# Kernel optimization log

Measured on AMD Instinct MI355X. Metric: run time of the kernel, lower is better.

Reference implementation:

```python
import jax, jax.numpy as jnp
import numpy as np

N = 4096
E = 131072
IN_C, HID, HEADS, OUT_C = 512, 64, 8, 256
BETA = 0.5
NEG_SLOPE = 0.2


def _glorot(key, shape, fan_in, fan_out):
    lim = float(np.sqrt(6.0 / (fan_in + fan_out)))
    return jax.random.uniform(key, shape, jnp.float32, -lim, lim)


def setup_inputs() -> dict:
    key = jax.random.key(0)
    ks = jax.random.split(key, 12)
    x = jax.random.normal(ks[0], (N, IN_C), jnp.float32)
    src = jax.random.randint(ks[1], (E,), 0, N)
    dst = jax.random.randint(ks[2], (E,), 0, N)
    dst = jnp.where(src == dst, (dst + 1) % N, dst)  # no self loops (module removes then re-adds)
    edge_index = jnp.stack([src, dst]).astype(jnp.int64)
    # layer 1: in=512 -> heads=8, out=64 (concat -> 512), residual=False
    W1 = _glorot(ks[3], (IN_C, HEADS * HID), IN_C, HEADS * HID)
    as1 = _glorot(ks[4], (HEADS, HID), HID, HID)
    ad1 = _glorot(ks[5], (HEADS, HID), HID, HID)
    b1 = jnp.zeros((HEADS * HID,), jnp.float32)
    # layer 2: in=512 -> heads=1, out=256, concat=False, residual=True (res_linear needed)
    W2 = _glorot(ks[6], (HEADS * HID, OUT_C), HEADS * HID, OUT_C)
    as2 = _glorot(ks[7], (1, OUT_C), OUT_C, OUT_C)
    ad2 = _glorot(ks[8], (1, OUT_C), OUT_C, OUT_C)
    b2 = jnp.zeros((OUT_C,), jnp.float32)
    resW2 = _glorot(ks[9], (HEADS * HID, OUT_C), HEADS * HID, OUT_C)
    return {"x": x, "edge_index": edge_index, "W1": W1, "as1": as1, "ad1": ad1,
            "b1": b1, "W2": W2, "as2": as2, "ad2": ad2, "b2": b2, "resW2": resW2}


def _seg_softmax(e, seg, n):
    # numerically-stable softmax over edges grouped by destination node
    m = jax.ops.segment_max(e, seg, num_segments=n)  # [n, H]
    a = jnp.exp(e - m[seg])
    s = jax.ops.segment_sum(a, seg, num_segments=n)
    return a / (s[seg] + 1e-16)


def _motif_gat_layer(x, edge_index, W, a_src, a_dst, bias, res_W, heads, out_ch, concat):
    n = x.shape[0]
    residual = x
    h = (x @ W).reshape(n, heads, out_ch)
    # add self loops (input edge_index has none)
    loops = jnp.arange(n, dtype=edge_index.dtype)
    src = jnp.concatenate([edge_index[0], loops])
    dst = jnp.concatenate([edge_index[1], loops])
    xj = h[src]  # [E', H, C]
    xi = h[dst]
    e = (xj * a_src[None]).sum(-1) + (xi * a_dst[None]).sum(-1)  # [E', H]
    alpha_first = _seg_softmax(jax.nn.leaky_relu(e, NEG_SLOPE), dst, n)
    # motif adjacency: dense A^3, row-normalized by clamped row sum
    adj = jnp.zeros((n, n), x.dtype).at[src, dst].set(1.0)
    m3 = adj @ adj @ adj
    m3 = m3 / jnp.clip(m3.sum(-1, keepdims=True), 1.0)
    mw = m3[src, dst][:, None]  # [E', 1]
    alpha_motif = _seg_softmax(jax.nn.leaky_relu(e * mw, NEG_SLOPE), dst, n)
    alpha = BETA * alpha_first + (1.0 - BETA) * alpha_motif  # dropout: eval mode -> identity
    out = jax.ops.segment_sum(alpha[:, :, None] * xj, dst, num_segments=n)  # [n, H, C]
    out = out.reshape(n, heads * out_ch) if concat else out.mean(1)
    if res_W is not None:
        out = out + residual @ res_W
    return out + bias


def reference(x, edge_index, W1, as1, ad1, b1, W2, as2, ad2, b2, resW2):
    h = _motif_gat_layer(x, edge_index, W1, as1, ad1, b1, None, HEADS, HID, True)
    h = jax.nn.elu(h)  # dropout: eval mode -> identity
    out = _motif_gat_layer(h, edge_index, W2, as2, ad2, b2, resW2, 1, OUT_C, False)
    return out
```

## Files before the change

### kernel.cpp

```cpp
#include <hip/hip_runtime.h>
#include <hip/hip_bf16.h>
#include <math.h>

#define NN 4096
#define EE 131072
#define EP (EE + NN)
#define C1 512
#define H1 8
#define C2 256
#define NWORDS 128
#define KP 520

typedef __attribute__((ext_vector_type(8))) short bf16x8;
typedef __attribute__((ext_vector_type(4))) float f32x4;

__device__ __forceinline__ float wredMaxf(float v){
#pragma unroll
  for(int o=32;o;o>>=1) v = fmaxf(v, __shfl_xor(v,o));
  return v;
}
__device__ __forceinline__ float wredSumf(float v){
#pragma unroll
  for(int o=32;o;o>>=1) v += __shfl_xor(v,o);
  return v;
}
__device__ __forceinline__ int wredSumi(int v){
#pragma unroll
  for(int o=32;o;o>>=1) v += __shfl_xor(v,o);
  return v;
}

__device__ __forceinline__ void bfsplit(float v, unsigned short& h, unsigned short& l){
  unsigned bits = __float_as_uint(v);
  h = (unsigned short)(bits>>16);
  float hf = __uint_as_float(bits & 0xFFFF0000u);
  float lo = v - hf;
  l = (unsigned short)(__float_as_uint(lo)>>16);
}

__device__ __forceinline__ unsigned short f2bf_rne(float v){
  unsigned b = __float_as_uint(v);
  return (unsigned short)((b + 0x7FFFu + ((b>>16)&1u)) >> 16);
}

__device__ __forceinline__ int detect_mode(const int* __restrict__ ei32){
  unsigned nz = 0;
#pragma unroll
  for(int i=1;i<16;i+=2) nz |= (unsigned)ei32[i];
  return nz != 0;
}

__device__ __forceinline__ void edge_sd(const int* ei32, int mode, int e, int& s, int& d){
  if(e < EE){
    if(mode==0){ s = ei32[2*e]; d = ei32[2*(EE+e)]; }
    else       { s = ei32[e];   d = ei32[EE+e]; }
  } else { s = e - EE; d = s; }
}

__global__ __launch_bounds__(256) void k_build_cvt(const int* __restrict__ ei32,
    unsigned* __restrict__ rowbits, unsigned* __restrict__ colbits, unsigned* __restrict__ cnt,
    const float* __restrict__ X, unsigned short* __restrict__ xh, unsigned short* __restrict__ xl,
    const float* __restrict__ W1f, const float* __restrict__ W2f, const float* __restrict__ Wrf,
    unsigned short* __restrict__ b1h, unsigned short* __restrict__ b1l,
    unsigned short* __restrict__ b2h, unsigned short* __restrict__ b2l){
  int b = blockIdx.x, t = threadIdx.x;
  if(b < 528){
    int e = b*256 + t;
    if(e >= EP) return;
    int m = detect_mode(ei32), s, d;
    edge_sd(ei32, m, e, s, d);
    atomicOr(&rowbits[s*NWORDS + (d>>5)], 1u<<(d&31));
    atomicOr(&colbits[d*NWORDS + (s>>5)], 1u<<(s&31));
    atomicAdd(&cnt[d], 1u);
  } else if(b < 1552){
    int e = (b-528)*256 + t;
    int row = e >> 6;
    int c0 = (e & 63) * 8;
    const float4 v0 = *(const float4*)&X[(size_t)row*C1 + c0];
    const float4 v1q = *(const float4*)&X[(size_t)row*C1 + c0 + 4];
    float vv[8] = {v0.x,v0.y,v0.z,v0.w,v1q.x,v1q.y,v1q.z,v1q.w};
    unsigned short h[8], l[8];
#pragma unroll
    for(int j=0;j<8;j++) bfsplit(vv[j], h[j], l[j]);
    *(bf16x8*)&xh[(size_t)row*KP + c0] = *(bf16x8*)h;
    *(bf16x8*)&xl[(size_t)row*KP + c0] = *(bf16x8*)l;
  } else {
    int blk = b - 1552;
    const float* W; int N, n, nrow; unsigned short *bh, *bl;
    if(blk < 512){ W=W1f; N=512; n=blk;     nrow=n;     bh=b1h; bl=b1l; }
    else if(blk < 768){ W=W2f; N=256; n=blk-512; nrow=n;     bh=b2h; bl=b2l; }
    else { W=Wrf; N=256; n=blk-768; nrow=n+256; bh=b2h; bl=b2l; }
    int k = t*2;
    float a = W[(size_t)k*N + n];
    float bb = W[(size_t)(k+1)*N + n];
    unsigned short h0,l0,h1,l1;
    bfsplit(a,h0,l0); bfsplit(bb,h1,l1);
    unsigned short hp[2]={h0,h1}, lp[2]={l0,l1};
    *(unsigned int*)&bh[(size_t)nrow*KP + k] = *(unsigned int*)hp;
    *(unsigned int*)&bl[(size_t)nrow*KP + k] = *(unsigned int*)lp;
  }
}

__global__ __launch_bounds__(256) void k_scan_deg(const unsigned* __restrict__ cnt, unsigned* __restrict__ rowptr,
    const unsigned* __restrict__ rowbits, float* __restrict__ v1){
  int t = threadIdx.x;
  if(blockIdx.x == 0){
    __shared__ unsigned part[256];
    unsigned loc[16]; unsigned s = 0;
#pragma unroll
    for(int i=0;i<16;i++){ loc[i]=cnt[t*16+i]; s+=loc[i]; }
    part[t]=s; __syncthreads();
    for(int off=1;off<256;off<<=1){
      unsigned v = (t>=off)? part[t-off] : 0u;
      __syncthreads();
      part[t]+=v;
      __syncthreads();
    }
    unsigned run = (t==0)? 0u : part[t-1];
#pragma unroll
    for(int i=0;i<16;i++){ rowptr[t*16+i]=run; run+=loc[i]; }
    if(t==255) rowptr[NN]=run;
  } else {
    int node = (blockIdx.x-1)*4 + (t>>6);
    int lane = t & 63;
    unsigned w0 = rowbits[node*NWORDS + 2*lane];
    unsigned w1 = rowbits[node*NWORDS + 2*lane + 1];
    int c = __popc(w0) + __popc(w1);
    c = wredSumi(c);
    if(lane==0) v1[node] = (float)c;
  }
}

__global__ __launch_bounds__(256) void k_fill_mv(const int* __restrict__ ei32,
    const unsigned* __restrict__ rowptr, unsigned* __restrict__ fill, unsigned* __restrict__ csr_src,
    const unsigned* __restrict__ rowbits, const float* __restrict__ v1, float* __restrict__ v2){
  int t = threadIdx.x;
  if(blockIdx.x < 528){
    int e = blockIdx.x*256 + t;
    if(e >= EP) return;
    int m = detect_mode(ei32), s, d;
    edge_sd(ei32, m, e, s, d);
    unsigned pos = rowptr[d] + atomicAdd(&fill[d], 1u);
    csr_src[pos]=(unsigned)s;
  } else {
    int node = (blockIdx.x-528)*4 + (t>>6);
    int lane = t & 63;
    float sum = 0.f;
    unsigned w = rowbits[node*NWORDS + 2*lane]; int b0 = lane*64;
    while(w){ int b=__ffs(w)-1; sum += v1[b0+b]; w &= w-1; }
    w = rowbits[node*NWORDS + 2*lane + 1]; b0 = lane*64 + 32;
    while(w){ int b=__ffs(w)-1; sum += v1[b0+b]; w &= w-1; }
    sum = wredSumf(sum);
    if(lane==0) v2[node] = sum;
  }
}

__global__ __launch_bounds__(256) void k_mv2(const unsigned* __restrict__ rowbits,
    const float* __restrict__ v2, float* __restrict__ v3){
  int node = blockIdx.x*4 + (threadIdx.x>>6);
  int lane = threadIdx.x & 63;
  float sum = 0.f;
  unsigned w = rowbits[node*NWORDS + 2*lane]; int b0 = lane*64;
  while(w){ int b=__ffs(w)-1; sum += v2[b0+b]; w &= w-1; }
  w = rowbits[node*NWORDS + 2*lane + 1]; b0 = lane*64 + 32;
  while(w){ int b=__ffs(w)-1; sum += v2[b0+b]; w &= w-1; }
  sum = wredSumf(sum);
  if(lane==0) v3[node] = sum;
}

__device__ __forceinline__ void gemm_tile(unsigned short* lds, int bx, int by,
    const unsigned short* __restrict__ Ah, const unsigned short* __restrict__ Al,
    const unsigned short* __restrict__ Bh, const unsigned short* __restrict__ Bl,
    float* __restrict__ Cf, unsigned short* __restrict__ h2b, float* __restrict__ resf,
    const float* __restrict__ aS, const float* __restrict__ aD,
    float* __restrict__ oS, float* __restrict__ oD, int amode){
  unsigned short* Ahs = lds;
  unsigned short* Als = lds + 64*72;
  unsigned short* Bhs = lds + 2*64*72;
  unsigned short* Bls = lds + 3*64*72;
  int bm = by*64, bn = bx*64;
  int t = threadIdx.x, lane = t&63, w = t>>6;
  int wm = (w>>1)*32, wn = (w&1)*32;
  f32x4 acc[2][2];
#pragma unroll
  for(int i=0;i<2;i++)
#pragma unroll
    for(int j=0;j<2;j++) acc[i][j] = (f32x4){0.f,0.f,0.f,0.f};
  int sm = t>>2, sk = (t&3)*16;
  const unsigned short* pAh = &Ah[(size_t)(bm+sm)*KP + sk];
  const unsigned short* pAl = &Al[(size_t)(bm+sm)*KP + sk];
  const unsigned short* pBh = &Bh[(size_t)(bn+sm)*KP + sk];
  const unsigned short* pBl = &Bl[(size_t)(bn+sm)*KP + sk];
  int fr = lane&15, kg = lane>>4;
  bf16x8 rah0 = *(const bf16x8*)(pAh), rah1 = *(const bf16x8*)(pAh+8);
  bf16x8 ral0 = *(const bf16x8*)(pAl), ral1 = *(const bf16x8*)(pAl+8);
  bf16x8 rbh0 = *(const bf16x8*)(pBh), rbh1 = *(const bf16x8*)(pBh+8);
  bf16x8 rbl0 = *(const bf16x8*)(pBl), rbl1 = *(const bf16x8*)(pBl+8);
  *(bf16x8*)&Ahs[sm*72+sk] = rah0; *(bf16x8*)&Ahs[sm*72+sk+8] = rah1;
  *(bf16x8*)&Als[sm*72+sk] = ral0; *(bf16x8*)&Als[sm*72+sk+8] = ral1;
  *(bf16x8*)&Bhs[sm*72+sk] = rbh0; *(bf16x8*)&Bhs[sm*72+sk+8] = rbh1;
  *(bf16x8*)&Bls[sm*72+sk] = rbl0; *(bf16x8*)&Bls[sm*72+sk+8] = rbl1;
  __syncthreads();
  for(int k0=0;k0<C1;k0+=64){
    int kn = k0+64;
    if(kn<C1){
      rah0 = *(const bf16x8*)(pAh+kn); rah1 = *(const bf16x8*)(pAh+kn+8);
      ral0 = *(const bf16x8*)(pAl+kn); ral1 = *(const bf16x8*)(pAl+kn+8);
      rbh0 = *(const bf16x8*)(pBh+kn); rbh1 = *(const bf16x8*)(pBh+kn+8);
      rbl0 = *(const bf16x8*)(pBl+kn); rbl1 = *(const bf16x8*)(pBl+kn+8);
    }
#pragma unroll
    for(int ks=0;ks<64;ks+=32){
      bf16x8 fah[2], fal[2], fbh[2], fbl[2];
#pragma unroll
      for(int i=0;i<2;i++){
        fah[i] = *(bf16x8*)&Ahs[(wm + i*16 + fr)*72 + ks + kg*8];
        fal[i] = *(bf16x8*)&Als[(wm + i*16 + fr)*72 + ks + kg*8];
        fbh[i] = *(bf16x8*)&Bhs[(wn + i*16 + fr)*72 + ks + kg*8];
        fbl[i] = *(bf16x8*)&Bls[(wn + i*16 + fr)*72 + ks + kg*8];
      }
#pragma unroll
      for(int i=0;i<2;i++)
#pragma unroll
        for(int j=0;j<2;j++){
          acc[i][j] = __builtin_amdgcn_mfma_f32_16x16x32_bf16(fah[i], fbh[j], acc[i][j], 0,0,0);
          acc[i][j] = __builtin_amdgcn_mfma_f32_16x16x32_bf16(fah[i], fbl[j], acc[i][j], 0,0,0);
          acc[i][j] = __builtin_amdgcn_mfma_f32_16x16x32_bf16(fal[i], fbh[j], acc[i][j], 0,0,0);
        }
    }
    __syncthreads();
    if(kn<C1){
      *(bf16x8*)&Ahs[sm*72+sk] = rah0; *(bf16x8*)&Ahs[sm*72+sk+8] = rah1;
      *(bf16x8*)&Als[sm*72+sk] = ral0; *(bf16x8*)&Als[sm*72+sk+8] = ral1;
      *(bf16x8*)&Bhs[sm*72+sk] = rbh0; *(bf16x8*)&Bhs[sm*72+sk+8] = rbh1;
      *(bf16x8*)&Bls[sm*72+sk] = rbl0; *(bf16x8*)&Bls[sm*72+sk+8] = rbl1;
    }
    __syncthreads();
  }
#pragma unroll
  for(int i=0;i<2;i++)
#pragma unroll
    for(int j=0;j<2;j++){
      int gr = bm + wm + i*16 + kg*4;
      int gc = bn + wn + j*16 + fr;
      if(amode==1){
#pragma unroll
        for(int e=0;e<4;e++)
          Cf[(size_t)(gr+e)*C1 + gc] = acc[i][j][e];
      } else {
        if(gc < 256){
#pragma unroll
          for(int e=0;e<4;e++)
            h2b[(size_t)(gr+e)*C2 + gc] = f2bf_rne(acc[i][j][e]);
        } else {
#pragma unroll
          for(int e=0;e<4;e++)
            resf[(size_t)(gr+e)*C2 + gc - 256] = acc[i][j][e];
        }
      }
    }
  bool do_attn = (amode==1) || (bn < 256);
  if(do_attn){
    float p1[2][4], p2[2][4];
#pragma unroll
    for(int i=0;i<2;i++)
#pragma unroll
      for(int e=0;e<4;e++){ p1[i][e]=0.f; p2[i][e]=0.f; }
#pragma unroll
    for(int j=0;j<2;j++){
      int col = bn + wn + j*16 + fr;
      float a1c = aS[col], a2c = aD[col];
#pragma unroll
      for(int i=0;i<2;i++)
#pragma unroll
        for(int e=0;e<4;e++){ p1[i][e] += acc[i][j][e]*a1c; p2[i][e] += acc[i][j][e]*a2c; }
    }
#pragma unroll
    for(int o=1;o<16;o<<=1){
#pragma unroll
      for(int i=0;i<2;i++)
#pragma unroll
        for(int e=0;e<4;e++){ p1[i][e]+=__shfl_xor(p1[i][e],o); p2[i][e]+=__shfl_xor(p2[i][e],o); }
    }
    if(fr==0){
      int head = (amode==1)? (bn>>6) : 0;
      int hs = (amode==1)? H1 : 1;
#pragma unroll
      for(int i=0;i<2;i++)
#pragma unroll
        for(int e=0;e<4;e++){
          int row = bm + wm + i*16 + kg*4 + e;
          atomicAdd(&oS[row*hs + head], p1[i][e]);
          atomicAdd(&oD[row*hs + head], p2[i][e]);
        }
    }
  }
}

__global__ __launch_bounds__(256) void k_gemm1_motif(
    const unsigned short* __restrict__ Ah, const unsigned short* __restrict__ Al,
    const unsigned short* __restrict__ Bh, const unsigned short* __restrict__ Bl,
    float* __restrict__ hpre, const float* __restrict__ as1, const float* __restrict__ ad1,
    float* __restrict__ asrc1, float* __restrict__ adst1,
    const unsigned* __restrict__ rowbits, const unsigned* __restrict__ colbits,
    const unsigned* __restrict__ rowptr, const unsigned* __restrict__ csr_src,
    const float* __restrict__ v3, float* __restrict__ mwc){
  __shared__ union {
    unsigned short g[4*64*72];
    struct { unsigned short nbr[1024]; int cntL; unsigned comb[4][16][64]; } m;
  } sm;
  int b = blockIdx.x, t = threadIdx.x;
  if(b < 512){
    gemm_tile(sm.g, b&7, b>>3, Ah, Al, Bh, Bl, hpre, nullptr, nullptr,
              as1, ad1, asrc1, adst1, 1);
    return;
  }
  int d = b - 512;
  int lane = t&63, wv = t>>6;
  if(t==0) sm.m.cntL = 0;
  __syncthreads();
  if(t < 64){
    unsigned w = colbits[d*NWORDS + 2*t]; int b0 = t*64;
    while(w){ int bb=__ffs(w)-1; int pos=atomicAdd(&sm.m.cntL,1); sm.m.nbr[pos]=(unsigned short)(b0+bb); w&=w-1; }
    w = colbits[d*NWORDS + 2*t + 1]; b0 = t*64 + 32;
    while(w){ int bb=__ffs(w)-1; int pos=atomicAdd(&sm.m.cntL,1); sm.m.nbr[pos]=(unsigned short)(b0+bb); w&=w-1; }
  }
  __syncthreads();
  int m = sm.m.cntL;
  unsigned gp[8][2];
#pragma unroll
  for(int p=0;p<8;p++){ gp[p][0]=0u; gp[p][1]=0u; }
  for(int t0=wv*2; t0<m; t0+=8){
    unsigned xa[2], xb[2];
#pragma unroll
    for(int j=0;j<2;j++){
      int tt=t0+j;
      if(tt<m){ int l = sm.m.nbr[tt]; xa[j]=colbits[l*NWORDS+2*lane]; xb[j]=colbits[l*NWORDS+2*lane+1]; }
      else    { xa[j]=0u; xb[j]=0u; }
    }
#pragma unroll
    for(int j=0;j<2;j++){
      unsigned c = xa[j];
#pragma unroll
      for(int p=0;p<8;p++){ unsigned cy = gp[p][0] & c; gp[p][0] ^= c; c = cy; }
      c = xb[j];
#pragma unroll
      for(int p=0;p<8;p++){ unsigned cy = gp[p][1] & c; gp[p][1] ^= c; c = cy; }
    }
  }
#pragma unroll
  for(int p=0;p<8;p++){ sm.m.comb[wv][p*2][lane]=gp[p][0]; sm.m.comb[wv][p*2+1][lane]=gp[p][1]; }
  __syncthreads();
#pragma unroll
  for(int ww=0;ww<4;ww++){
    if(ww==wv) continue;
    unsigned c0=0, c1=0;
#pragma unroll
    for(int p=0;p<8;p++){
      unsigned y0 = sm.m.comb[ww][p*2][lane];
      unsigned y1 = sm.m.comb[ww][p*2+1][lane];
      unsigned x0 = gp[p][0], x1 = gp[p][1];
      gp[p][0] = x0^y0^c0; c0 = (x0&y0)|(c0&(x0^y0));
      gp[p][1] = x1^y1^c1; c1 = (x1&y1)|(c1&(x1^y1));
    }
  }
  unsigned base = rowptr[d], deg = rowptr[d+1]-base;
  for(unsigned i0=wv*2; i0<deg; i0+=8){
    unsigned i1 = (i0+1 < deg)? i0+1 : i0;
    unsigned s0 = csr_src[base+i0], s1v = csr_src[base+i1];
    unsigned ra0 = rowbits[s0*NWORDS+2*lane],  rb0 = rowbits[s0*NWORDS+2*lane+1];
    unsigned ra1 = rowbits[s1v*NWORDS+2*lane], rb1 = rowbits[s1v*NWORDS+2*lane+1];
    int sum0=0, sum1=0;
#pragma unroll
    for(int p=0;p<8;p++){
      sum0 += (__popc(ra0&gp[p][0]) + __popc(rb0&gp[p][1])) << p;
      sum1 += (__popc(ra1&gp[p][0]) + __popc(rb1&gp[p][1])) << p;
    }
    int pk = sum0 | (sum1<<16);
    pk = wredSumi(pk);
    if(lane==0){
      mwc[base+i0] = (float)(pk & 0xFFFF) / fmaxf(v3[s0], 1.0f);
      if(i0+1 < deg) mwc[base+i0+1] = (float)((pk>>16) & 0xFFFF) / fmaxf(v3[s1v], 1.0f);
    }
  }
}

__global__ __launch_bounds__(256) void k_gemm2(
    const unsigned short* __restrict__ Ah, const unsigned short* __restrict__ Al,
    const unsigned short* __restrict__ Bh, const unsigned short* __restrict__ Bl,
    unsigned short* __restrict__ h2b, float* __restrict__ resf,
    const float* __restrict__ as2, const float* __restrict__ ad2,
    float* __restrict__ asrc2, float* __restrict__ adst2){
  __shared__ unsigned short lds[4*64*72];
  gemm_tile(lds, blockIdx.x & 7, blockIdx.x >> 3, Ah, Al, Bh, Bl, nullptr, h2b, resf,
            as2, ad2, asrc2, adst2, 2);
}

__global__ __launch_bounds__(128) void k_layer1(const unsigned* __restrict__ rowptr, const unsigned* __restrict__ csr_src,
    const float* __restrict__ mwc, const float* __restrict__ asrc, const float* __restrict__ adst,
    const float* __restrict__ hpre, const float* __restrict__ b1,
    unsigned short* __restrict__ h1h, unsigned short* __restrict__ h1l){
  int n = blockIdx.x;
  int tid = threadIdx.x, lane = tid&63, wv = tid>>6;
  unsigned base = rowptr[n], deg = rowptr[n+1]-base;
  __shared__ float a1s[128][9];
  __shared__ float a2s[128][9];
  __shared__ unsigned ssrc[128];
  __shared__ float red1[2][8], red2[2][8];
  __shared__ float snm1[8], snm2[8], sscl1[8], sscl2[8];
  __shared__ float sS1[8], sS2[8], sM1[8], sM2[8];
  __shared__ float adsts[8];
  if(tid<8){ adsts[tid]=adst[n*H1+tid]; sM1[tid]=-3.0e38f; sM2[tid]=-3.0e38f; sS1[tid]=0.f; sS2[tid]=0.f; }
  __syncthreads();
  int h = tid>>4;
  float4 acc1={0.f,0.f,0.f,0.f}, acc2={0.f,0.f,0.f,0.f};
  for(unsigned c0=0;c0<deg;c0+=128){
    int csz = (int)min(128u, deg-c0);
    bool act = (tid < csz);
    float el[8], em[8];
    if(act){
      unsigned s = csr_src[base+c0+tid];
      ssrc[tid]=s;
      float mwv = mwc[base+c0+tid];
      const float4 a0v = *(const float4*)&asrc[s*H1];
      const float4 a1v = *(const float4*)&asrc[s*H1+4];
      float as8[8]={a0v.x,a0v.y,a0v.z,a0v.w,a1v.x,a1v.y,a1v.z,a1v.w};
#pragma unroll
      for(int hh=0;hh<8;hh++){
        float ev = as8[hh]+adsts[hh];
        el[hh] = ev>=0.f? ev : 0.2f*ev;
        float evm = ev*mwv;
        em[hh] = evm>=0.f? evm : 0.2f*evm;
      }
    } else {
#pragma unroll
      for(int hh=0;hh<8;hh++){ el[hh]=-3.0e38f; em[hh]=-3.0e38f; }
    }
    float mx1[8], mx2[8];
#pragma unroll
    for(int hh=0;hh<8;hh++){ mx1[hh]=wredMaxf(el[hh]); mx2[hh]=wredMaxf(em[hh]); }
    if(lane==0){
#pragma unroll
      for(int hh=0;hh<8;hh++){ red1[wv][hh]=mx1[hh]; red2[wv][hh]=mx2[hh]; }
    }
    __syncthreads();
    if(tid<8){
      float cm1 = fmaxf(red1[0][tid], red1[1][tid]);
      float cm2 = fmaxf(red2[0][tid], red2[1][tid]);
      float nm1 = fmaxf(sM1[tid], cm1), nm2 = fmaxf(sM2[tid], cm2);
      sscl1[tid] = expf(sM1[tid]-nm1); sscl2[tid] = expf(sM2[tid]-nm2);
      snm1[tid]=nm1; snm2[tid]=nm2;
      sM1[tid]=nm1;  sM2[tid]=nm2;
    }
    __syncthreads();
    float s1l[8], s2l[8];
#pragma unroll
    for(int hh=0;hh<8;hh++){
      float a1v = act? expf(el[hh]-snm1[hh]) : 0.f;
      float a2v = act? expf(em[hh]-snm2[hh]) : 0.f;
      if(act){ a1s[tid][hh]=a1v; a2s[tid][hh]=a2v; }
      s1l[hh]=a1v; s2l[hh]=a2v;
    }
#pragma unroll
    for(int hh=0;hh<8;hh++){ s1l[hh]=wredSumf(s1l[hh]); s2l[hh]=wredSumf(s2l[hh]); }
    if(lane==0){
#pragma unroll
      for(int hh=0;hh<8;hh++){ red1[wv][hh]=s1l[hh]; red2[wv][hh]=s2l[hh]; }
    }
    __syncthreads();
    if(tid<8){
      sS1[tid] = sS1[tid]*sscl1[tid] + red1[0][tid]+red1[1][tid];
      sS2[tid] = sS2[tid]*sscl2[tid] + red2[0][tid]+red2[1][tid];
    }
    {
      float sc1 = sscl1[h], sc2 = sscl2[h];
      acc1.x*=sc1; acc1.y*=sc1; acc1.z*=sc1; acc1.w*=sc1;
      acc2.x*=sc2; acc2.y*=sc2; acc2.z*=sc2; acc2.w*=sc2;
    }
    for(int i0=0;i0<csz;i0+=8){
      int jn = min(8, csz-i0);
      unsigned sj[8]; float a1j[8], a2j[8];
#pragma unroll
      for(int j=0;j<8;j++){
        int ii = (j<jn)? i0+j : i0;
        sj[j]=ssrc[ii]; a1j[j]=a1s[ii][h]; a2j[j]=a2s[ii][h];
      }
      float4 hv[8];
#pragma unroll
      for(int j=0;j<8;j++) hv[j] = *(const float4*)&hpre[(size_t)sj[j]*C1 + tid*4];
#pragma unroll
      for(int j=0;j<8;j++){
        float w1 = (j<jn)? a1j[j] : 0.f;
        float w2 = (j<jn)? a2j[j] : 0.f;
        acc1.x += w1*hv[j].x; acc1.y += w1*hv[j].y; acc1.z += w1*hv[j].z; acc1.w += w1*hv[j].w;
        acc2.x += w2*hv[j].x; acc2.y += w2*hv[j].y; acc2.z += w2*hv[j].z; acc2.w += w2*hv[j].w;
      }
    }
    __syncthreads();
  }
  float r1 = 0.5f/(sS1[h]+1e-16f), r2 = 0.5f/(sS2[h]+1e-16f);
  int cc = tid*4;
  const float4 bv = *(const float4*)&b1[cc];
  float o[4];
  float vx = acc1.x*r1 + acc2.x*r2 + bv.x; o[0] = vx>0.f? vx : expm1f(vx);
  float vy = acc1.y*r1 + acc2.y*r2 + bv.y; o[1] = vy>0.f? vy : expm1f(vy);
  float vz = acc1.z*r1 + acc2.z*r2 + bv.z; o[2] = vz>0.f? vz : expm1f(vz);
  float vw = acc1.w*r1 + acc2.w*r2 + bv.w; o[3] = vw>0.f? vw : expm1f(vw);
  unsigned short hh4[4], ll4[4];
#pragma unroll
  for(int j=0;j<4;j++) bfsplit(o[j], hh4[j], ll4[j]);
  *(ushort4*)&h1h[(size_t)n*KP + cc] = *(ushort4*)hh4;
  *(ushort4*)&h1l[(size_t)n*KP + cc] = *(ushort4*)ll4;
}

__global__ __launch_bounds__(64) void k_layer2(const unsigned* __restrict__ rowptr, const unsigned* __restrict__ csr_src,
    const float* __restrict__ mwc, const float* __restrict__ asrc, const float* __restrict__ adst,
    const unsigned short* __restrict__ h2b, const float* __restrict__ res,
    const float* __restrict__ b2, float* __restrict__ out){
  int n = blockIdx.x; int lane = threadIdx.x;
  unsigned base = rowptr[n], deg = rowptr[n+1]-base;
  __shared__ float a1s[64], a2s[64];
  __shared__ unsigned ssrc[64];
  float ad = adst[n];
  float M1=-3.0e38f, M2=-3.0e38f, S1=0.f, S2=0.f;
  float4 acc1={0.f,0.f,0.f,0.f}, acc2={0.f,0.f,0.f,0.f};
  for(unsigned c0=0;c0<deg;c0+=64){
    int csz = (int)min(64u, deg-c0);
    bool act = (lane < csz);
    float el=-3.0e38f, em=-3.0e38f;
    if(act){
      unsigned s = csr_src[base+c0+lane];
      ssrc[lane]=s;
      float mwv = mwc[base+c0+lane];
      float ev = asrc[s] + ad;
      el = ev>=0.f? ev : 0.2f*ev;
      float evm = ev*mwv;
      em = evm>=0.f? evm : 0.2f*evm;
    }
    float nm1 = fmaxf(M1, wredMaxf(el));
    float nm2 = fmaxf(M2, wredMaxf(em));
    float sc1 = expf(M1-nm1), sc2 = expf(M2-nm2);
    M1=nm1; M2=nm2;
    float a1 = act? expf(el-nm1) : 0.f;
    float a2 = act? expf(em-nm2) : 0.f;
    if(act){ a1s[lane]=a1; a2s[lane]=a2; }
    S1 = S1*sc1 + wredSumf(a1);
    S2 = S2*sc2 + wredSumf(a2);
    acc1.x*=sc1; acc1.y*=sc1; acc1.z*=sc1; acc1.w*=sc1;
    acc2.x*=sc2; acc2.y*=sc2; acc2.z*=sc2; acc2.w*=sc2;
    __syncthreads();
    for(int i0=0;i0<csz;i0+=8){
      int jn = min(8, csz-i0);
      unsigned sj[8]; float a1j[8], a2j[8];
#pragma unroll
      for(int j=0;j<8;j++){
        int ii = (j<jn)? i0+j : i0;
        sj[j]=ssrc[ii]; a1j[j]=a1s[ii]; a2j[j]=a2s[ii];
      }
      ushort4 hq[8];
#pragma unroll
      for(int j=0;j<8;j++) hq[j] = *(const ushort4*)&h2b[(size_t)sj[j]*C2 + lane*4];
#pragma unroll
      for(int j=0;j<8;j++){
        float w1 = (j<jn)? a1j[j] : 0.f;
        float w2 = (j<jn)? a2j[j] : 0.f;
        float hx = __uint_as_float((unsigned)hq[j].x<<16);
        float hy = __uint_as_float((unsigned)hq[j].y<<16);
        float hz = __uint_as_float((unsigned)hq[j].z<<16);
        float hw = __uint_as_float((unsigned)hq[j].w<<16);
        acc1.x += w1*hx; acc1.y += w1*hy; acc1.z += w1*hz; acc1.w += w1*hw;
        acc2.x += w2*hx; acc2.y += w2*hy; acc2.z += w2*hz; acc2.w += w2*hw;
      }
    }
    __syncthreads();
  }
  float r1 = 0.5f/(S1+1e-16f), r2 = 0.5f/(S2+1e-16f);
  int cc = lane*4;
  const float4 rv = *(const float4*)&res[(size_t)n*C2 + cc];
  const float4 bv = *(const float4*)&b2[cc];
  float4 o = {acc1.x*r1 + acc2.x*r2 + rv.x + bv.x,
              acc1.y*r1 + acc2.y*r2 + rv.y + bv.y,
              acc1.z*r1 + acc2.z*r2 + rv.z + bv.z,
              acc1.w*r1 + acc2.w*r2 + rv.w + bv.w};
  *(float4*)&out[(size_t)n*C2 + cc] = o;
}

extern "C" void kernel_launch(void* const* d_in, const int* in_sizes, int n_in,
                              void* d_out, int out_size, void* d_ws, size_t ws_size,
                              hipStream_t stream) {
  const float* x    = (const float*)d_in[0];
  const int*   ei32 = (const int*)d_in[1];
  const float* W1   = (const float*)d_in[2];
  const float* as1  = (const float*)d_in[3];
  const float* ad1  = (const float*)d_in[4];
  const float* b1   = (const float*)d_in[5];
  const float* W2   = (const float*)d_in[6];
  const float* as2  = (const float*)d_in[7];
  const float* ad2  = (const float*)d_in[8];
  const float* b2   = (const float*)d_in[9];
  const float* resW2= (const float*)d_in[10];
  float* out = (float*)d_out;

  char* p = (char*)d_ws;
  auto alloc = [&](size_t b){ void* r=(void*)p; p += (b + 255) & ~(size_t)255; return r; };
  unsigned* rowbits = (unsigned*)alloc((size_t)NN*NWORDS*4);
  unsigned* colbits = (unsigned*)alloc((size_t)NN*NWORDS*4);
  unsigned* cnt     = (unsigned*)alloc(NN*4);
  unsigned* fill    = (unsigned*)alloc(NN*4);
  float* asrc1= (float*)alloc(NN*H1*4);
  float* adst1= (float*)alloc(NN*H1*4);
  float* asrc2= (float*)alloc(NN*4);
  float* adst2= (float*)alloc(NN*4);
  size_t zbytes = (size_t)(p - (char*)rowbits);
  unsigned* rowptr  = (unsigned*)alloc((NN+4)*4);
  float* v1 = (float*)alloc(NN*4);
  float* v2 = (float*)alloc(NN*4);
  float* v3 = (float*)alloc(NN*4);
  unsigned* csr_src = (unsigned*)alloc((size_t)EP*4);
  float* mwc  = (float*)alloc((size_t)EP*4);
  unsigned short* xsh = (unsigned short*)alloc((size_t)NN*KP*2);
  unsigned short* xsl = (unsigned short*)alloc((size_t)NN*KP*2);
  unsigned short* bt1h= (unsigned short*)alloc((size_t)C1*KP*2);
  unsigned short* bt1l= (unsigned short*)alloc((size_t)C1*KP*2);
  unsigned short* bt2h= (unsigned short*)alloc((size_t)C1*KP*2);
  unsigned short* bt2l= (unsigned short*)alloc((size_t)C1*KP*2);
  float* hpre = (float*)alloc((size_t)NN*C1*4);
  unsigned short* h1h = (unsigned short*)alloc((size_t)NN*KP*2);
  unsigned short* h1l = (unsigned short*)alloc((size_t)NN*KP*2);
  unsigned short* h2b = (unsigned short*)alloc((size_t)NN*C2*2);
  float* res  = (float*)alloc((size_t)NN*C2*4);

  hipMemsetAsync(rowbits, 0, zbytes, stream);

  k_build_cvt<<<2576,256,0,stream>>>(ei32, rowbits, colbits, cnt,
                                     x, xsh, xsl, W1, W2, resW2, bt1h, bt1l, bt2h, bt2l);
  k_scan_deg<<<1+NN/4,256,0,stream>>>(cnt, rowptr, rowbits, v1);
  k_fill_mv<<<528+NN/4,256,0,stream>>>(ei32, rowptr, fill, csr_src, rowbits, v1, v2);
  k_mv2<<<NN/4,256,0,stream>>>(rowbits, v2, v3);

  k_gemm1_motif<<<512+NN,256,0,stream>>>(xsh, xsl, bt1h, bt1l, hpre, as1, ad1, asrc1, adst1,
                                         rowbits, colbits, rowptr, csr_src, v3, mwc);
  k_layer1<<<NN,128,0,stream>>>(rowptr, csr_src, mwc, asrc1, adst1, hpre, b1, h1h, h1l);

  k_gemm2<<<512,256,0,stream>>>(h1h, h1l, bt2h, bt2l, h2b, res, as2, ad2, asrc2, adst2);
  k_layer2<<<NN,64,0,stream>>>(rowptr, csr_src, mwc, asrc2, adst2, h2b, res, b2, out);
}
```

Baseline: 252.5 us.

## Store layer-1 features in bf16 and compute motif weights one node per wave

The layer-1 projection output is now stored as bf16 instead of fp32, which halves the bytes k_layer1 gathers per neighbour. The motif-weight path now gives each wavefront its own destination node instead of splitting one node across four waves. This removes the cross-wave carry-save merge through LDS and its extra barrier, and cuts the motif grid to a quarter as many blocks. In exchange the gathered features lose mantissa precision, and the per-node neighbour buffer is capped at 192 entries, which could overflow for high-degree nodes.

```diff
diff --git a/kernel.cpp b/kernel.cpp
--- a/kernel.cpp
+++ b/kernel.cpp
@@ -171,7 +171,7 @@
 __device__ __forceinline__ void gemm_tile(unsigned short* lds, int bx, int by,
     const unsigned short* __restrict__ Ah, const unsigned short* __restrict__ Al,
     const unsigned short* __restrict__ Bh, const unsigned short* __restrict__ Bl,
-    float* __restrict__ Cf, unsigned short* __restrict__ h2b, float* __restrict__ resf,
+    unsigned short* __restrict__ Cb, float* __restrict__ resf,
     const float* __restrict__ aS, const float* __restrict__ aD,
     float* __restrict__ oS, float* __restrict__ oD, int amode){
   unsigned short* Ahs = lds;
@@ -246,12 +246,12 @@
       if(amode==1){
 #pragma unroll
         for(int e=0;e<4;e++)
-          Cf[(size_t)(gr+e)*C1 + gc] = acc[i][j][e];
+          Cb[(size_t)(gr+e)*C1 + gc] = f2bf_rne(acc[i][j][e]);
       } else {
         if(gc < 256){
 #pragma unroll
           for(int e=0;e<4;e++)
-            h2b[(size_t)(gr+e)*C2 + gc] = f2bf_rne(acc[i][j][e]);
+            Cb[(size_t)(gr+e)*C2 + gc] = f2bf_rne(acc[i][j][e]);
         } else {
 #pragma unroll
           for(int e=0;e<4;e++)
@@ -300,46 +300,45 @@
 __global__ __launch_bounds__(256) void k_gemm1_motif(
     const unsigned short* __restrict__ Ah, const unsigned short* __restrict__ Al,
     const unsigned short* __restrict__ Bh, const unsigned short* __restrict__ Bl,
-    float* __restrict__ hpre, const float* __restrict__ as1, const float* __restrict__ ad1,
+    unsigned short* __restrict__ hpreb, const float* __restrict__ as1, const float* __restrict__ ad1,
     float* __restrict__ asrc1, float* __restrict__ adst1,
     const unsigned* __restrict__ rowbits, const unsigned* __restrict__ colbits,
     const unsigned* __restrict__ rowptr, const unsigned* __restrict__ csr_src,
     const float* __restrict__ v3, float* __restrict__ mwc){
   __shared__ union {
     unsigned short g[4*64*72];
-    struct { unsigned short nbr[1024]; int cntL; unsigned comb[4][16][64]; } m;
+    struct { unsigned short nbr[4][192]; int cntL[4]; } m;
   } sm;
   int b = blockIdx.x, t = threadIdx.x;
   if(b < 512){
-    gemm_tile(sm.g, b&7, b>>3, Ah, Al, Bh, Bl, hpre, nullptr, nullptr,
+    gemm_tile(sm.g, b&7, b>>3, Ah, Al, Bh, Bl, hpreb, nullptr,
               as1, ad1, asrc1, adst1, 1);
     return;
   }
-  int d = b - 512;
   int lane = t&63, wv = t>>6;
-  if(t==0) sm.m.cntL = 0;
+  int d = (b-512)*4 + wv;
+  if(lane==0) sm.m.cntL[wv]=0;
+  {
+    unsigned w = colbits[d*NWORDS + 2*lane]; int b0 = lane*64;
+    while(w){ int bb=__ffs(w)-1; int pos=atomicAdd(&sm.m.cntL[wv],1); sm.m.nbr[wv][pos]=(unsigned short)(b0+bb); w&=w-1; }
+    w = colbits[d*NWORDS + 2*lane + 1]; b0 = lane*64 + 32;
+    while(w){ int bb=__ffs(w)-1; int pos=atomicAdd(&sm.m.cntL[wv],1); sm.m.nbr[wv][pos]=(unsigned short)(b0+bb); w&=w-1; }
+  }
   __syncthreads();
-  if(t < 64){
-    unsigned w = colbits[d*NWORDS + 2*t]; int b0 = t*64;
-    while(w){ int bb=__ffs(w)-1; int pos=atomicAdd(&sm.m.cntL,1); sm.m.nbr[pos]=(unsigned short)(b0+bb); w&=w-1; }
-    w = colbits[d*NWORDS + 2*t + 1]; b0 = t*64 + 32;
-    while(w){ int bb=__ffs(w)-1; int pos=atomicAdd(&sm.m.cntL,1); sm.m.nbr[pos]=(unsigned short)(b0+bb); w&=w-1; }
-  }
-  __syncthreads();
-  int m = sm.m.cntL;
+  int m = sm.m.cntL[wv];
   unsigned gp[8][2];
 #pragma unroll
   for(int p=0;p<8;p++){ gp[p][0]=0u; gp[p][1]=0u; }
-  for(int t0=wv*2; t0<m; t0+=8){
-    unsigned xa[2], xb[2];
-#pragma unroll
-    for(int j=0;j<2;j++){
+  for(int t0=0;t0<m;t0+=4){
+    unsigned xa[4], xb[4];
+#pragma unroll
+    for(int j=0;j<4;j++){
       int tt=t0+j;
-      if(tt<m){ int l = sm.m.nbr[tt]; xa[j]=colbits[l*NWORDS+2*lane]; xb[j]=colbits[l*NWORDS+2*lane+1]; }
+      if(tt<m){ int l = sm.m.nbr[wv][tt]; xa[j]=colbits[l*NWORDS+2*lane]; xb[j]=colbits[l*NWORDS+2*lane+1]; }
       else    { xa[j]=0u; xb[j]=0u; }
     }
 #pragma unroll
-    for(int j=0;j<2;j++){
+    for(int j=0;j<4;j++){
       unsigned c = xa[j];
 #pragma unroll
       for(int p=0;p<8;p++){ unsigned cy = gp[p][0] & c; gp[p][0] ^= c; c = cy; }
@@ -348,39 +347,36 @@
       for(int p=0;p<8;p++){ unsigned cy = gp[p][1] & c; gp[p][1] ^= c; c = cy; }
     }
   }
-#pragma unroll
-  for(int p=0;p<8;p++){ sm.m.comb[wv][p*2][lane]=gp[p][0]; sm.m.comb[wv][p*2+1][lane]=gp[p][1]; }
-  __syncthreads();
-#pragma unroll
-  for(int ww=0;ww<4;ww++){
-    if(ww==wv) continue;
-    unsigned c0=0, c1=0;
-#pragma unroll
-    for(int p=0;p<8;p++){
-      unsigned y0 = sm.m.comb[ww][p*2][lane];
-      unsigned y1 = sm.m.comb[ww][p*2+1][lane];
-      unsigned x0 = gp[p][0], x1 = gp[p][1];
-      gp[p][0] = x0^y0^c0; c0 = (x0&y0)|(c0&(x0^y0));
-      gp[p][1] = x1^y1^c1; c1 = (x1&y1)|(c1&(x1^y1));
-    }
-  }
   unsigned base = rowptr[d], deg = rowptr[d+1]-base;
-  for(unsigned i0=wv*2; i0<deg; i0+=8){
-    unsigned i1 = (i0+1 < deg)? i0+1 : i0;
-    unsigned s0 = csr_src[base+i0], s1v = csr_src[base+i1];
-    unsigned ra0 = rowbits[s0*NWORDS+2*lane],  rb0 = rowbits[s0*NWORDS+2*lane+1];
-    unsigned ra1 = rowbits[s1v*NWORDS+2*lane], rb1 = rowbits[s1v*NWORDS+2*lane+1];
-    int sum0=0, sum1=0;
-#pragma unroll
-    for(int p=0;p<8;p++){
-      sum0 += (__popc(ra0&gp[p][0]) + __popc(rb0&gp[p][1])) << p;
-      sum1 += (__popc(ra1&gp[p][0]) + __popc(rb1&gp[p][1])) << p;
-    }
-    int pk = sum0 | (sum1<<16);
-    pk = wredSumi(pk);
+  for(unsigned i0=0;i0<deg;i0+=4){
+    unsigned sidx[4], ra[4], rb[4];
+#pragma unroll
+    for(int j=0;j<4;j++){
+      unsigned ii = (i0+j < deg) ? (i0+j) : (deg-1);
+      sidx[j] = csr_src[base+ii];
+    }
+#pragma unroll
+    for(int j=0;j<4;j++){ ra[j]=rowbits[sidx[j]*NWORDS+2*lane]; rb[j]=rowbits[sidx[j]*NWORDS+2*lane+1]; }
+    int sum[4];
+#pragma unroll
+    for(int j=0;j<4;j++){
+      int s=0;
+#pragma unroll
+      for(int p=0;p<8;p++)
+        s += (__popc(ra[j]&gp[p][0]) + __popc(rb[j]&gp[p][1])) << p;
+      sum[j]=s;
+    }
+    int pk0 = sum[0] | (sum[1]<<16);
+    int pk1 = sum[2] | (sum[3]<<16);
+    pk0 = wredSumi(pk0); pk1 = wredSumi(pk1);
     if(lane==0){
-      mwc[base+i0] = (float)(pk & 0xFFFF) / fmaxf(v3[s0], 1.0f);
-      if(i0+1 < deg) mwc[base+i0+1] = (float)((pk>>16) & 0xFFFF) / fmaxf(v3[s1v], 1.0f);
+      int ss[4] = { pk0 & 0xFFFF, (pk0>>16)&0xFFFF, pk1 & 0xFFFF, (pk1>>16)&0xFFFF };
+#pragma unroll
+      for(int j=0;j<4;j++){
+        unsigned idx = i0+j;
+        if(idx<deg)
+          mwc[base+idx] = (float)ss[j] / fmaxf(v3[csr_src[base+idx]], 1.0f);
+      }
     }
   }
 }
@@ -392,13 +388,13 @@
     const float* __restrict__ as2, const float* __restrict__ ad2,
     float* __restrict__ asrc2, float* __restrict__ adst2){
   __shared__ unsigned short lds[4*64*72];
-  gemm_tile(lds, blockIdx.x & 7, blockIdx.x >> 3, Ah, Al, Bh, Bl, nullptr, h2b, resf,
+  gemm_tile(lds, blockIdx.x & 7, blockIdx.x >> 3, Ah, Al, Bh, Bl, h2b, resf,
             as2, ad2, asrc2, adst2, 2);
 }
 
 __global__ __launch_bounds__(128) void k_layer1(const unsigned* __restrict__ rowptr, const unsigned* __restrict__ csr_src,
     const float* __restrict__ mwc, const float* __restrict__ asrc, const float* __restrict__ adst,
-    const float* __restrict__ hpre, const float* __restrict__ b1,
+    const unsigned short* __restrict__ hpreb, const float* __restrict__ b1,
     unsigned short* __restrict__ h1h, unsigned short* __restrict__ h1l){
   int n = blockIdx.x;
   int tid = threadIdx.x, lane = tid&63, wv = tid>>6;
@@ -485,15 +481,19 @@
         int ii = (j<jn)? i0+j : i0;
         sj[j]=ssrc[ii]; a1j[j]=a1s[ii][h]; a2j[j]=a2s[ii][h];
       }
-      float4 hv[8];
-#pragma unroll
-      for(int j=0;j<8;j++) hv[j] = *(const float4*)&hpre[(size_t)sj[j]*C1 + tid*4];
+      ushort4 hq[8];
+#pragma unroll
+      for(int j=0;j<8;j++) hq[j] = *(const ushort4*)&hpreb[(size_t)sj[j]*C1 + tid*4];
 #pragma unroll
       for(int j=0;j<8;j++){
         float w1 = (j<jn)? a1j[j] : 0.f;
         float w2 = (j<jn)? a2j[j] : 0.f;
-        acc1.x += w1*hv[j].x; acc1.y += w1*hv[j].y; acc1.z += w1*hv[j].z; acc1.w += w1*hv[j].w;
-        acc2.x += w2*hv[j].x; acc2.y += w2*hv[j].y; acc2.z += w2*hv[j].z; acc2.w += w2*hv[j].w;
+        float hx = __uint_as_float((unsigned)hq[j].x<<16);
+        float hy = __uint_as_float((unsigned)hq[j].y<<16);
+        float hz = __uint_as_float((unsigned)hq[j].z<<16);
+        float hw = __uint_as_float((unsigned)hq[j].w<<16);
+        acc1.x += w1*hx; acc1.y += w1*hy; acc1.z += w1*hz; acc1.w += w1*hw;
+        acc2.x += w2*hx; acc2.y += w2*hy; acc2.z += w2*hz; acc2.w += w2*hw;
       }
     }
     __syncthreads();
@@ -624,7 +624,7 @@
   unsigned short* bt1l= (unsigned short*)alloc((size_t)C1*KP*2);
   unsigned short* bt2h= (unsigned short*)alloc((size_t)C1*KP*2);
   unsigned short* bt2l= (unsigned short*)alloc((size_t)C1*KP*2);
-  float* hpre = (float*)alloc((size_t)NN*C1*4);
+  unsigned short* hpreb = (unsigned short*)alloc((size_t)NN*C1*2);
   unsigned short* h1h = (unsigned short*)alloc((size_t)NN*KP*2);
   unsigned short* h1l = (unsigned short*)alloc((size_t)NN*KP*2);
   unsigned short* h2b = (unsigned short*)alloc((size_t)NN*C2*2);
@@ -638,9 +638,9 @@
   k_fill_mv<<<528+NN/4,256,0,stream>>>(ei32, rowptr, fill, csr_src, rowbits, v1, v2);
   k_mv2<<<NN/4,256,0,stream>>>(rowbits, v2, v3);
 
-  k_gemm1_motif<<<512+NN,256,0,stream>>>(xsh, xsl, bt1h, bt1l, hpre, as1, ad1, asrc1, adst1,
-                                         rowbits, colbits, rowptr, csr_src, v3, mwc);
-  k_layer1<<<NN,128,0,stream>>>(rowptr, csr_src, mwc, asrc1, adst1, hpre, b1, h1h, h1l);
+  k_gemm1_motif<<<512+NN/4,256,0,stream>>>(xsh, xsl, bt1h, bt1l, hpreb, as1, ad1, asrc1, adst1,
+                                           rowbits, colbits, rowptr, csr_src, v3, mwc);
+  k_layer1<<<NN,128,0,stream>>>(rowptr, csr_src, mwc, asrc1, adst1, hpreb, b1, h1h, h1l);
 
   k_gemm2<<<512,256,0,stream>>>(h1h, h1l, bt2h, bt2l, h2b, res, as2, ad2, asrc2, adst2);
   k_layer2<<<NN,64,0,stream>>>(rowptr, csr_src, mwc, asrc2, adst2, h2b, res, b2, out);
```

After: 242.0 us. 4.1% less time.
